# Performance work log

Measured on AMD Instinct MI355X. Metric: run time of the kernel, lower is better.

Reference implementation:

```python
import jax, jax.numpy as jnp
import numpy as np

H = 16  # n_heads


def setup_inputs() -> dict:
    key = jax.random.key(0)
    ks = jax.random.split(key, 12)
    B, S, D = 16, 512, 1024
    inp = {
        "query": jax.random.normal(ks[0], (B, S, D), jnp.float32),
        "key": jax.random.normal(ks[1], (B, S, D), jnp.float32),
        "value": jax.random.normal(ks[2], (B, S, D), jnp.float32),
        "mask": jnp.ones((B, S), dtype=bool),
        "adj": jax.random.uniform(ks[3], (B, S, S), jnp.float32),
        # nn.Linear weights are [out, in]; y = x @ W.T + b
        "Wq": jax.random.normal(ks[4], (D, D), jnp.float32) / np.sqrt(D),
        "bq": jnp.zeros((D,), jnp.float32),
        "Wk": jax.random.normal(ks[5], (D, D), jnp.float32) / np.sqrt(D),
        "bk": jnp.zeros((D,), jnp.float32),
        "Wv": jax.random.normal(ks[6], (D, D), jnp.float32) / np.sqrt(D),
        "bv": jnp.zeros((D,), jnp.float32),
        "Wo": jax.random.normal(ks[7], (D, D), jnp.float32) / np.sqrt(D),
        "bo": jnp.zeros((D,), jnp.float32),
        "beta": jnp.array([0.5], jnp.float32),  # learned residual scale (init 0 in torch)
    }
    return inp


def reference(query, key, value, mask, adj, Wq, bq, Wk, bk, Wv, bv, Wo, bo, beta):
    B, S, D = query.shape
    h = H
    dk = D // h
    N = S * dk  # channel-attention "sequence" length

    def proj(x, W, b):
        # [B,S,D] -> [B,h,S,dk]
        return (x @ W.T + b).reshape(B, S, h, dk).transpose(0, 2, 1, 3)

    Q = proj(query, Wq, bq)
    K = proj(key, Wk, bk)
    V = proj(value, Wv, bv)

    # Flatten each head: [B, h, S*dk]; torch's q,k,v are the [B,N,h] transposes.
    Qf = Q.reshape(B, h, N)
    Kf = K.reshape(B, h, N)
    Vf = V.reshape(B, h, N)

    # channel attention: scores = q^T k / sqrt(h) -> [B,h,h]
    scores = jnp.einsum("bin,bjn->bij", Qf, Kf) / jnp.sqrt(jnp.asarray(h, Qf.dtype))
    attn = jax.nn.softmax(scores, axis=-1)  # dropout is identity at eval

    # x2 = attn @ v^T -> [B,h,N] -> view [B,h,S,dk]
    x2 = jnp.einsum("bij,bjn->bin", attn, Vf).reshape(B, h, S, dk)

    x = V + beta * x2                      # scaled residual on value
    x = x.transpose(0, 2, 1, 3).reshape(B, S, D)
    out = x @ Wo.T + bo
    return out, attn
```

## Files before the change

kernel.cpp:

```cpp
#include <hip/hip_runtime.h>
#include <cstdint>
#include <cstddef>


#define DIM 1024

typedef _Float16 f16_t;
typedef _Float16 f16x4_t __attribute__((ext_vector_type(4)));
typedef _Float16 f16x8_t __attribute__((ext_vector_type(8)));
typedef float    f32x4_t __attribute__((ext_vector_type(4)));

__device__ __forceinline__ void async_ld16(const void* g, void* l) {
    __builtin_amdgcn_global_load_lds((const __attribute__((address_space(1))) void*)g,
                                     (__attribute__((address_space(3))) void*)l,
                                     16, 0, 0);
}

__global__ __launch_bounds__(256) void pack_kernel(
    const float* __restrict__ q, const float* __restrict__ k, const float* __restrict__ v,
    const float* __restrict__ Wq, const float* __restrict__ Wk,
    const float* __restrict__ Wv, const float* __restrict__ Wo,
    f16_t* __restrict__ Aq, f16_t* __restrict__ Ak, f16_t* __restrict__ Av,
    f16_t* __restrict__ Bq, f16_t* __restrict__ Bk,
    f16_t* __restrict__ Bv, f16_t* __restrict__ Bo,
    float* __restrict__ scores)
{
    const int u = blockIdx.x * 256 + threadIdx.x;
    if (u >= 7340032) {
        scores[u - 7340032] = 0.f;
        return;
    }
    const float* src; f16_t* dst; int i;
    if (u < 2097152)      { src = q;  dst = Aq; i = u; }
    else if (u < 4194304) { src = k;  dst = Ak; i = u - 2097152; }
    else if (u < 6291456) { src = v;  dst = Av; i = u - 4194304; }
    else if (u < 6553600) { src = Wq; dst = Bq; i = u - 6291456; }
    else if (u < 6815744) { src = Wk; dst = Bk; i = u - 6553600; }
    else if (u < 7077888) { src = Wv; dst = Bv; i = u - 6815744; }
    else                  { src = Wo; dst = Bo; i = u - 7077888; }
    float4 s = ((const float4*)src)[i];
    f16x4_t h;
    h[0] = (f16_t)s.x; h[1] = (f16_t)s.y; h[2] = (f16_t)s.z; h[3] = (f16_t)s.w;
    ((f16x4_t*)dst)[i] = h;
}

__device__ __forceinline__ void gemm_body(
    const f16_t* __restrict__ A, const f16_t* __restrict__ B,
    const float* __restrict__ bias, float* __restrict__ C, f16_t* __restrict__ C16,
    f16_t* As, f16_t* Bs, int tileM, int tileN)
{
    const int tid  = threadIdx.x;
    const int lane = tid & 63;
    const int w    = tid >> 6;
    const int wm = (w & 1) << 6;
    const int wn = (w >> 1) << 6;

    f32x4_t acc[4][4];
#pragma unroll
    for (int i = 0; i < 4; ++i)
#pragma unroll
        for (int j = 0; j < 4; ++j)
            acc[i][j] = (f32x4_t){0.f, 0.f, 0.f, 0.f};

    const int srow = lane >> 3;
    const int scol = ((lane & 7) ^ (lane >> 3)) << 3;
    const int arow = lane & 15;
    const int sx   = lane & 7;
    const int kqu  = lane >> 4;

    for (int kt = 0; kt < 16; ++kt) {
        const int k0 = kt << 6;
#pragma unroll
        for (int t = 0; t < 4; ++t) {
            const int row = (w << 5) + (t << 3);
            async_ld16(A + (size_t)(tileM + row + srow) * DIM + k0 + scol,
                       (void*)(As + row * 64));
            async_ld16(B + (size_t)(tileN + row + srow) * DIM + k0 + scol,
                       (void*)(Bs + row * 64));
        }
        __syncthreads();
#pragma unroll
        for (int kk = 0; kk < 2; ++kk) {
            const int cu = ((kk << 2) + kqu) ^ sx;
            f16x8_t af[4], bfv[4];
#pragma unroll
            for (int mt = 0; mt < 4; ++mt)
                af[mt] = *(const f16x8_t*)(As + (wm + (mt << 4) + arow) * 64 + (cu << 3));
#pragma unroll
            for (int nt = 0; nt < 4; ++nt)
                bfv[nt] = *(const f16x8_t*)(Bs + (wn + (nt << 4) + arow) * 64 + (cu << 3));
#pragma unroll
            for (int mt = 0; mt < 4; ++mt)
#pragma unroll
                for (int nt = 0; nt < 4; ++nt)
                    acc[mt][nt] = __builtin_amdgcn_mfma_f32_16x16x32_f16(
                        af[mt], bfv[nt], acc[mt][nt], 0, 0, 0);
        }
        __syncthreads();
    }

    const int rq = (lane >> 4) << 2;
    if (C16) {
#pragma unroll
        for (int nt = 0; nt < 4; ++nt) {
            const int col = tileN + wn + (nt << 4) + arow;
            const float bv = bias[col];
#pragma unroll
            for (int mt = 0; mt < 4; ++mt) {
                const int row = tileM + wm + (mt << 4) + rq;
#pragma unroll
                for (int r = 0; r < 4; ++r)
                    C16[(size_t)(row + r) * DIM + col] = (f16_t)(acc[mt][nt][r] + bv);
            }
        }
    } else {
#pragma unroll
        for (int nt = 0; nt < 4; ++nt) {
            const int col = tileN + wn + (nt << 4) + arow;
            const float bv = bias[col];
#pragma unroll
            for (int mt = 0; mt < 4; ++mt) {
                const int row = tileM + wm + (mt << 4) + rq;
#pragma unroll
                for (int r = 0; r < 4; ++r)
                    C[(size_t)(row + r) * DIM + col] = acc[mt][nt][r] + bv;
            }
        }
    }
}

struct Gemm3Args {
    const f16_t* A[3];
    const f16_t* B[3];
    const float* bias[3];
    float*       C[3];
    f16_t*       C16[3];
};

__global__ __launch_bounds__(256) void gemm3(Gemm3Args args)
{
    __shared__ __align__(16) f16_t As[128 * 64];
    __shared__ __align__(16) f16_t Bs[128 * 64];
    const int z = blockIdx.z;
    gemm_body(args.A[z], args.B[z], args.bias[z], args.C[z], args.C16[z],
              As, Bs, blockIdx.x * 128, blockIdx.y * 128);
}

__global__ __launch_bounds__(256) void gemm_f16(
    const f16_t* __restrict__ A, const f16_t* __restrict__ B,
    const float* __restrict__ bias, float* __restrict__ C)
{
    __shared__ __align__(16) f16_t As[128 * 64];
    __shared__ __align__(16) f16_t Bs[128 * 64];
    gemm_body(A, B, bias, C, nullptr, As, Bs, blockIdx.x * 128, blockIdx.y * 128);
}

__global__ __launch_bounds__(256) void scores_kernel(
    const f16_t* __restrict__ Pq16, const f16_t* __restrict__ Pk16,
    float* __restrict__ scores)
{
    __shared__ float red[4][256];
    const int b = blockIdx.x;
    const int lane = threadIdx.x & 63;
    const int w = threadIdx.x >> 6;
    const int m  = lane & 15;
    const int q8 = (lane >> 4) << 3;

    f32x4_t acc = (f32x4_t){0.f, 0.f, 0.f, 0.f};
    const int s0 = blockIdx.y * 16 + w * 4;
#pragma unroll
    for (int ss = 0; ss < 4; ++ss) {
        const size_t rb = (size_t)(b * 512 + s0 + ss) * DIM;
        const f16_t* qrow = Pq16 + rb;
        const f16_t* krow = Pk16 + rb;
#pragma unroll
        for (int c0 = 0; c0 < 64; c0 += 32) {
            f16x8_t af = *(const f16x8_t*)(qrow + m * 64 + c0 + q8);
            f16x8_t bf = *(const f16x8_t*)(krow + m * 64 + c0 + q8);
            acc = __builtin_amdgcn_mfma_f32_16x16x32_f16(af, bf, acc, 0, 0, 0);
        }
    }
    const int rq = (lane >> 4) << 2;
#pragma unroll
    for (int r = 0; r < 4; ++r)
        red[w][(rq + r) * 16 + m] = acc[r];
    __syncthreads();
    const int t = threadIdx.x;
    const float sum = red[0][t] + red[1][t] + red[2][t] + red[3][t];
    atomicAdd(&scores[b * 256 + t], sum);
}

__global__ __launch_bounds__(256) void softmax_kernel(
    const float* __restrict__ scores, const float* __restrict__ beta_p,
    float* __restrict__ attn_out, float* __restrict__ Mm)
{
    const int t = threadIdx.x;
    const int i = t & 15;
    const float beta = beta_p[0];
    float s[16];
    float mx = -1e30f;
#pragma unroll
    for (int j = 0; j < 16; ++j) {
        s[j] = scores[t * 16 + j] * 0.25f;
        mx = fmaxf(mx, s[j]);
    }
    float sum = 0.f;
#pragma unroll
    for (int j = 0; j < 16; ++j) { s[j] = expf(s[j] - mx); sum += s[j]; }
    const float inv = 1.f / sum;
#pragma unroll
    for (int j = 0; j < 16; ++j) {
        float a = s[j] * inv;
        attn_out[t * 16 + j] = a;
        Mm[t * 16 + j] = beta * a + ((j == i) ? 1.f : 0.f);
    }
}

__global__ __launch_bounds__(256) void mix_kernel(
    const float* __restrict__ Pv, const float* __restrict__ Mm,
    f16_t* __restrict__ xmix)
{
    __shared__ float Msh[256];
    const int rbase = blockIdx.x * 8;
    const int b = rbase >> 9;
    Msh[threadIdx.x] = Mm[b * 256 + threadIdx.x];
    __syncthreads();
    const int w = threadIdx.x >> 6;
    const int lane = threadIdx.x & 63;
#pragma unroll
    for (int rr = 0; rr < 2; ++rr) {
        const int r = rbase + w * 2 + rr;
        const float* vrow = Pv + (size_t)r * DIM;
        float v[16];
#pragma unroll
        for (int j = 0; j < 16; ++j) v[j] = vrow[j * 64 + lane];
#pragma unroll
        for (int i = 0; i < 16; ++i) {
            float x = 0.f;
#pragma unroll
            for (int j = 0; j < 16; ++j) x += Msh[i * 16 + j] * v[j];
            xmix[(size_t)r * DIM + i * 64 + lane] = (f16_t)x;
        }
    }
}

extern "C" void kernel_launch(void* const* d_in, const int* in_sizes, int n_in,
                              void* d_out, int out_size, void* d_ws, size_t ws_size,
                              hipStream_t stream)
{
    (void)in_sizes; (void)n_in; (void)out_size; (void)ws_size;
    const float* q    = (const float*)d_in[0];
    const float* k    = (const float*)d_in[1];
    const float* v    = (const float*)d_in[2];
    const float* Wq   = (const float*)d_in[5];
    const float* bq   = (const float*)d_in[6];
    const float* Wk   = (const float*)d_in[7];
    const float* bk   = (const float*)d_in[8];
    const float* Wv   = (const float*)d_in[9];
    const float* bv   = (const float*)d_in[10];
    const float* Wo   = (const float*)d_in[11];
    const float* bo   = (const float*)d_in[12];
    const float* beta = (const float*)d_in[13];

    float* out  = (float*)d_out;
    float* attn = (float*)d_out + 8388608;

    char* p = (char*)d_ws;
    auto take = [&](size_t n) -> char* {
        char* cur = p; p += (n + 255) & ~(size_t)255; return cur;
    };
    f16_t* Aq = (f16_t*)take(16777216);
    f16_t* Ak = (f16_t*)take(16777216);
    f16_t* Av = (f16_t*)take(16777216);
    f16_t* Bq = (f16_t*)take(2097152);
    f16_t* Bk = (f16_t*)take(2097152);
    f16_t* Bv = (f16_t*)take(2097152);
    f16_t* Bo = (f16_t*)take(2097152);
    f16_t* Pq16 = (f16_t*)take(16777216);
    f16_t* Pk16 = (f16_t*)take(16777216);
    float* Pv = (float*)take(33554432);
    float* scores = (float*)take(16384);
    float* Mm     = (float*)take(16384);
    f16_t* xmix = Aq;

    pack_kernel<<<28688, 256, 0, stream>>>(q, k, v, Wq, Wk, Wv, Wo,
                                           Aq, Ak, Av, Bq, Bk, Bv, Bo, scores);

    Gemm3Args ga;
    ga.A[0] = Aq; ga.A[1] = Ak; ga.A[2] = Av;
    ga.B[0] = Bq; ga.B[1] = Bk; ga.B[2] = Bv;
    ga.bias[0] = bq; ga.bias[1] = bk; ga.bias[2] = bv;
    ga.C[0] = nullptr; ga.C[1] = nullptr; ga.C[2] = Pv;
    ga.C16[0] = Pq16; ga.C16[1] = Pk16; ga.C16[2] = nullptr;
    gemm3<<<dim3(64, 8, 3), 256, 0, stream>>>(ga);

    scores_kernel<<<dim3(16, 32), 256, 0, stream>>>(Pq16, Pk16, scores);
    softmax_kernel<<<1, 256, 0, stream>>>(scores, beta, attn, Mm);
    mix_kernel<<<1024, 256, 0, stream>>>(Pv, Mm, xmix);
    gemm_f16<<<dim3(64, 8), 256, 0, stream>>>(xmix, Bo, bo, out);
}
```

Measured before the change: 291.4 us.

## Fuse fp32-to-fp16 activation conversion into projection GEMM and softmax into mix

The projection GEMM now reads fp32 activations directly, converting them to fp16 in registers before storing to LDS, which removes the separate pack pass over q/k/v and its fp16 round-trip buffers. The V projection is stored as fp16 instead of fp32, halving its write and read traffic. Softmax is folded into the mix kernel, where each block recomputes its batch's 16x16 softmax, so the single-block softmax launch goes away. In exchange, A tiles now load synchronously instead of async-to-LDS, and V loses precision by being stored in fp16.

Result: no change. 292.2 us (+0.3%).

```diff
diff --git a/kernel.cpp b/kernel.cpp
--- a/kernel.cpp
+++ b/kernel.cpp
@@ -16,42 +16,143 @@
                                      16, 0, 0);
 }
 
-__global__ __launch_bounds__(256) void pack_kernel(
-    const float* __restrict__ q, const float* __restrict__ k, const float* __restrict__ v,
+__global__ __launch_bounds__(256) void pack_w_kernel(
     const float* __restrict__ Wq, const float* __restrict__ Wk,
     const float* __restrict__ Wv, const float* __restrict__ Wo,
-    f16_t* __restrict__ Aq, f16_t* __restrict__ Ak, f16_t* __restrict__ Av,
     f16_t* __restrict__ Bq, f16_t* __restrict__ Bk,
     f16_t* __restrict__ Bv, f16_t* __restrict__ Bo,
     float* __restrict__ scores)
 {
     const int u = blockIdx.x * 256 + threadIdx.x;
-    if (u >= 7340032) {
-        scores[u - 7340032] = 0.f;
+    if (u >= 1048576) {
+        scores[u - 1048576] = 0.f;
         return;
     }
     const float* src; f16_t* dst; int i;
-    if (u < 2097152)      { src = q;  dst = Aq; i = u; }
-    else if (u < 4194304) { src = k;  dst = Ak; i = u - 2097152; }
-    else if (u < 6291456) { src = v;  dst = Av; i = u - 4194304; }
-    else if (u < 6553600) { src = Wq; dst = Bq; i = u - 6291456; }
-    else if (u < 6815744) { src = Wk; dst = Bk; i = u - 6553600; }
-    else if (u < 7077888) { src = Wv; dst = Bv; i = u - 6815744; }
-    else                  { src = Wo; dst = Bo; i = u - 7077888; }
+    if (u < 262144)      { src = Wq; dst = Bq; i = u; }
+    else if (u < 524288) { src = Wk; dst = Bk; i = u - 262144; }
+    else if (u < 786432) { src = Wv; dst = Bv; i = u - 524288; }
+    else                 { src = Wo; dst = Bo; i = u - 786432; }
     float4 s = ((const float4*)src)[i];
     f16x4_t h;
     h[0] = (f16_t)s.x; h[1] = (f16_t)s.y; h[2] = (f16_t)s.z; h[3] = (f16_t)s.w;
     ((f16x4_t*)dst)[i] = h;
 }
 
-__device__ __forceinline__ void gemm_body(
-    const f16_t* __restrict__ A, const f16_t* __restrict__ B,
-    const float* __restrict__ bias, float* __restrict__ C, f16_t* __restrict__ C16,
-    f16_t* As, f16_t* Bs, int tileM, int tileN)
-{
+struct Gemm3Args {
+    const float* A[3];
+    const f16_t* B[3];
+    const float* bias[3];
+    f16_t*       C16[3];
+};
+
+__global__ __launch_bounds__(256) void gemm3(Gemm3Args args)
+{
+    __shared__ __align__(16) f16_t As[128 * 64];
+    __shared__ __align__(16) f16_t Bs[128 * 64];
+
+    const int z = blockIdx.z;
+    const float* __restrict__ A  = args.A[z];
+    const f16_t* __restrict__ B  = args.B[z];
+    const float* __restrict__ bias = args.bias[z];
+    f16_t* __restrict__ C16 = args.C16[z];
+
     const int tid  = threadIdx.x;
     const int lane = tid & 63;
     const int w    = tid >> 6;
+    const int tileM = blockIdx.x * 128;
+    const int tileN = blockIdx.y * 128;
+    const int wm = (w & 1) << 6;
+    const int wn = (w >> 1) << 6;
+
+    f32x4_t acc[4][4];
+#pragma unroll
+    for (int i = 0; i < 4; ++i)
+#pragma unroll
+        for (int j = 0; j < 4; ++j)
+            acc[i][j] = (f32x4_t){0.f, 0.f, 0.f, 0.f};
+
+    const int srow = lane >> 3;
+    const int u8   = lane & 7;
+    const int gcol = ((u8 ^ srow) << 3);
+    const int arow = lane & 15;
+    const int sx   = lane & 7;
+    const int kqu  = lane >> 4;
+
+    for (int kt = 0; kt < 16; ++kt) {
+        const int k0 = kt << 6;
+        float4 a0[4], a1[4];
+#pragma unroll
+        for (int t = 0; t < 4; ++t) {
+            const int row = (w << 5) + (t << 3) + srow;
+            const float* src = A + (size_t)(tileM + row) * DIM + k0 + gcol;
+            a0[t] = *(const float4*)(src);
+            a1[t] = *(const float4*)(src + 4);
+        }
+#pragma unroll
+        for (int t = 0; t < 4; ++t) {
+            const int rowb = (w << 5) + (t << 3);
+            async_ld16(B + (size_t)(tileN + rowb + srow) * DIM + k0 + gcol,
+                       (void*)(Bs + rowb * 64));
+        }
+#pragma unroll
+        for (int t = 0; t < 4; ++t) {
+            const int row = (w << 5) + (t << 3) + srow;
+            f16x8_t h;
+            h[0] = (f16_t)a0[t].x; h[1] = (f16_t)a0[t].y;
+            h[2] = (f16_t)a0[t].z; h[3] = (f16_t)a0[t].w;
+            h[4] = (f16_t)a1[t].x; h[5] = (f16_t)a1[t].y;
+            h[6] = (f16_t)a1[t].z; h[7] = (f16_t)a1[t].w;
+            *(f16x8_t*)(As + row * 64 + (u8 << 3)) = h;
+        }
+        __syncthreads();
+#pragma unroll
+        for (int kk = 0; kk < 2; ++kk) {
+            const int cu = ((kk << 2) + kqu) ^ sx;
+            f16x8_t af[4], bfv[4];
+#pragma unroll
+            for (int mt = 0; mt < 4; ++mt)
+                af[mt] = *(const f16x8_t*)(As + (wm + (mt << 4) + arow) * 64 + (cu << 3));
+#pragma unroll
+            for (int nt = 0; nt < 4; ++nt)
+                bfv[nt] = *(const f16x8_t*)(Bs + (wn + (nt << 4) + arow) * 64 + (cu << 3));
+#pragma unroll
+            for (int mt = 0; mt < 4; ++mt)
+#pragma unroll
+                for (int nt = 0; nt < 4; ++nt)
+                    acc[mt][nt] = __builtin_amdgcn_mfma_f32_16x16x32_f16(
+                        af[mt], bfv[nt], acc[mt][nt], 0, 0, 0);
+        }
+        __syncthreads();
+    }
+
+    const int rq = (lane >> 4) << 2;
+#pragma unroll
+    for (int nt = 0; nt < 4; ++nt) {
+        const int col = tileN + wn + (nt << 4) + arow;
+        const float bv = bias[col];
+#pragma unroll
+        for (int mt = 0; mt < 4; ++mt) {
+            const int row = tileM + wm + (mt << 4) + rq;
+#pragma unroll
+            for (int r = 0; r < 4; ++r)
+                C16[(size_t)(row + r) * DIM + col] = (f16_t)(acc[mt][nt][r] + bv);
+        }
+    }
+}
+
+__global__ __launch_bounds__(256) void gemm_out(
+    const f16_t* __restrict__ A, const f16_t* __restrict__ B,
+    const float* __restrict__ bias, float* __restrict__ C)
+{
+    __shared__ __align__(16) f16_t As[128 * 64];
+    __shared__ __align__(16) f16_t Bs[128 * 64];
+
+    const int tid  = threadIdx.x;
+    const int lane = tid & 63;
+    const int w    = tid >> 6;
+    const int tileM = blockIdx.x * 128;
+    const int tileN = blockIdx.y * 128;
     const int wm = (w & 1) << 6;
     const int wn = (w >> 1) << 6;
 
@@ -100,59 +201,18 @@
     }
 
     const int rq = (lane >> 4) << 2;
-    if (C16) {
-#pragma unroll
-        for (int nt = 0; nt < 4; ++nt) {
-            const int col = tileN + wn + (nt << 4) + arow;
-            const float bv = bias[col];
-#pragma unroll
-            for (int mt = 0; mt < 4; ++mt) {
-                const int row = tileM + wm + (mt << 4) + rq;
-#pragma unroll
-                for (int r = 0; r < 4; ++r)
-                    C16[(size_t)(row + r) * DIM + col] = (f16_t)(acc[mt][nt][r] + bv);
-            }
-        }
-    } else {
-#pragma unroll
-        for (int nt = 0; nt < 4; ++nt) {
-            const int col = tileN + wn + (nt << 4) + arow;
-            const float bv = bias[col];
-#pragma unroll
-            for (int mt = 0; mt < 4; ++mt) {
-                const int row = tileM + wm + (mt << 4) + rq;
-#pragma unroll
-                for (int r = 0; r < 4; ++r)
-                    C[(size_t)(row + r) * DIM + col] = acc[mt][nt][r] + bv;
-            }
-        }
-    }
-}
-
-struct Gemm3Args {
-    const f16_t* A[3];
-    const f16_t* B[3];
-    const float* bias[3];
-    float*       C[3];
-    f16_t*       C16[3];
-};
-
-__global__ __launch_bounds__(256) void gemm3(Gemm3Args args)
-{
-    __shared__ __align__(16) f16_t As[128 * 64];
-    __shared__ __align__(16) f16_t Bs[128 * 64];
-    const int z = blockIdx.z;
-    gemm_body(args.A[z], args.B[z], args.bias[z], args.C[z], args.C16[z],
-              As, Bs, blockIdx.x * 128, blockIdx.y * 128);
-}
-
-__global__ __launch_bounds__(256) void gemm_f16(
-    const f16_t* __restrict__ A, const f16_t* __restrict__ B,
-    const float* __restrict__ bias, float* __restrict__ C)
-{
-    __shared__ __align__(16) f16_t As[128 * 64];
-    __shared__ __align__(16) f16_t Bs[128 * 64];
-    gemm_body(A, B, bias, C, nullptr, As, Bs, blockIdx.x * 128, blockIdx.y * 128);
+#pragma unroll
+    for (int nt = 0; nt < 4; ++nt) {
+        const int col = tileN + wn + (nt << 4) + arow;
+        const float bv = bias[col];
+#pragma unroll
+        for (int mt = 0; mt < 4; ++mt) {
+            const int row = tileM + wm + (mt << 4) + rq;
+#pragma unroll
+            for (int r = 0; r < 4; ++r)
+                C[(size_t)(row + r) * DIM + col] = acc[mt][nt][r] + bv;
+        }
+    }
 }
 
 __global__ __launch_bounds__(256) void scores_kernel(
@@ -190,50 +250,46 @@
     atomicAdd(&scores[b * 256 + t], sum);
 }
 
-__global__ __launch_bounds__(256) void softmax_kernel(
+__global__ __launch_bounds__(256) void mix_kernel(
     const float* __restrict__ scores, const float* __restrict__ beta_p,
-    float* __restrict__ attn_out, float* __restrict__ Mm)
-{
-    const int t = threadIdx.x;
-    const int i = t & 15;
-    const float beta = beta_p[0];
-    float s[16];
-    float mx = -1e30f;
-#pragma unroll
-    for (int j = 0; j < 16; ++j) {
-        s[j] = scores[t * 16 + j] * 0.25f;
-        mx = fmaxf(mx, s[j]);
-    }
-    float sum = 0.f;
-#pragma unroll
-    for (int j = 0; j < 16; ++j) { s[j] = expf(s[j] - mx); sum += s[j]; }
-    const float inv = 1.f / sum;
-#pragma unroll
-    for (int j = 0; j < 16; ++j) {
-        float a = s[j] * inv;
-        attn_out[t * 16 + j] = a;
-        Mm[t * 16 + j] = beta * a + ((j == i) ? 1.f : 0.f);
-    }
-}
-
-__global__ __launch_bounds__(256) void mix_kernel(
-    const float* __restrict__ Pv, const float* __restrict__ Mm,
-    f16_t* __restrict__ xmix)
+    const f16_t* __restrict__ Pv16,
+    float* __restrict__ attn_out, f16_t* __restrict__ xmix)
 {
     __shared__ float Msh[256];
     const int rbase = blockIdx.x * 8;
     const int b = rbase >> 9;
-    Msh[threadIdx.x] = Mm[b * 256 + threadIdx.x];
+    const int t = threadIdx.x;
+    if (t < 16) {
+        const float beta = beta_p[0];
+        float s[16];
+        float mx = -1e30f;
+#pragma unroll
+        for (int j = 0; j < 16; ++j) {
+            s[j] = scores[b * 256 + t * 16 + j] * 0.25f;
+            mx = fmaxf(mx, s[j]);
+        }
+        float sum = 0.f;
+#pragma unroll
+        for (int j = 0; j < 16; ++j) { s[j] = __expf(s[j] - mx); sum += s[j]; }
+        const float inv = 1.f / sum;
+        const bool write_attn = (rbase & 511) == 0;
+#pragma unroll
+        for (int j = 0; j < 16; ++j) {
+            float a = s[j] * inv;
+            if (write_attn) attn_out[b * 256 + t * 16 + j] = a;
+            Msh[t * 16 + j] = beta * a + ((j == t) ? 1.f : 0.f);
+        }
+    }
     __syncthreads();
-    const int w = threadIdx.x >> 6;
-    const int lane = threadIdx.x & 63;
+    const int w = t >> 6;
+    const int lane = t & 63;
 #pragma unroll
     for (int rr = 0; rr < 2; ++rr) {
         const int r = rbase + w * 2 + rr;
-        const float* vrow = Pv + (size_t)r * DIM;
+        const f16_t* vrow = Pv16 + (size_t)r * DIM;
         float v[16];
 #pragma unroll
-        for (int j = 0; j < 16; ++j) v[j] = vrow[j * 64 + lane];
+        for (int j = 0; j < 16; ++j) v[j] = (float)vrow[j * 64 + lane];
 #pragma unroll
         for (int i = 0; i < 16; ++i) {
             float x = 0.f;
@@ -269,33 +325,27 @@
     auto take = [&](size_t n) -> char* {
         char* cur = p; p += (n + 255) & ~(size_t)255; return cur;
     };
-    f16_t* Aq = (f16_t*)take(16777216);
-    f16_t* Ak = (f16_t*)take(16777216);
-    f16_t* Av = (f16_t*)take(16777216);
     f16_t* Bq = (f16_t*)take(2097152);
     f16_t* Bk = (f16_t*)take(2097152);
     f16_t* Bv = (f16_t*)take(2097152);
     f16_t* Bo = (f16_t*)take(2097152);
     f16_t* Pq16 = (f16_t*)take(16777216);
     f16_t* Pk16 = (f16_t*)take(16777216);
-    float* Pv = (float*)take(33554432);
+    f16_t* Pv16 = (f16_t*)take(16777216);
+    f16_t* xmix = (f16_t*)take(16777216);
     float* scores = (float*)take(16384);
-    float* Mm     = (float*)take(16384);
-    f16_t* xmix = Aq;
-
-    pack_kernel<<<28688, 256, 0, stream>>>(q, k, v, Wq, Wk, Wv, Wo,
-                                           Aq, Ak, Av, Bq, Bk, Bv, Bo, scores);
+
+    pack_w_kernel<<<4112, 256, 0, stream>>>(Wq, Wk, Wv, Wo,
+                                            Bq, Bk, Bv, Bo, scores);
 
     Gemm3Args ga;
-    ga.A[0] = Aq; ga.A[1] = Ak; ga.A[2] = Av;
+    ga.A[0] = q;  ga.A[1] = k;  ga.A[2] = v;
     ga.B[0] = Bq; ga.B[1] = Bk; ga.B[2] = Bv;
     ga.bias[0] = bq; ga.bias[1] = bk; ga.bias[2] = bv;
-    ga.C[0] = nullptr; ga.C[1] = nullptr; ga.C[2] = Pv;
-    ga.C16[0] = Pq16; ga.C16[1] = Pk16; ga.C16[2] = nullptr;
+    ga.C16[0] = Pq16; ga.C16[1] = Pk16; ga.C16[2] = Pv16;
     gemm3<<<dim3(64, 8, 3), 256, 0, stream>>>(ga);
 
     scores_kernel<<<dim3(16, 32), 256, 0, stream>>>(Pq16, Pk16, scores);
-    softmax_kernel<<<1, 256, 0, stream>>>(scores, beta, attn, Mm);
-    mix_kernel<<<1024, 256, 0, stream>>>(Pv, Mm, xmix);
-    gemm_f16<<<dim3(64, 8), 256, 0, stream>>>(xmix, Bo, bo, out);
-}
+    mix_kernel<<<1024, 256, 0, stream>>>(scores, beta, Pv16, attn, xmix);
+    gemm_out<<<dim3(64, 8), 256, 0, stream>>>(xmix, Bo, bo, out);
+}
```
